# Performance work log

Measured on AMD Instinct MI355X. Metric: run time of the kernel, lower is better.

## Reference

```python
import jax, jax.numpy as jnp
import numpy as np

T, H, F, E, K = 4096, 2048, 1408, 8, 2  # tokens, hidden, intermediate, experts, top_k


def setup_inputs() -> dict:
    key = jax.random.key(0)
    k1, k2, k3, k4 = jax.random.split(key, 4)
    return {
        "hidden_states": jax.random.normal(k1, (T, H), dtype=jnp.float32),
        "router_logits": jax.random.normal(k2, (T, E), dtype=jnp.float32),
        # w1: (E, 2, H, F) where dim 1 = [gate_proj, up_proj]
        "w1": jax.random.normal(k3, (E, 2, H, F), dtype=jnp.float32) * 0.02,
        # w2: (E, F, H) down projection
        "w2": jax.random.normal(k4, (E, F, H), dtype=jnp.float32) * 0.02,
        "top_k": K,
    }


def reference(hidden_states, router_logits, w1, w2, top_k):
    # Router: softmax over all experts, then select top_k.
    # renormalize_topk_logits=False -> combine weights are the raw softmax probs.
    probs = jax.nn.softmax(router_logits, axis=-1)            # (T, E)
    topk_w, topk_ids = jax.lax.top_k(probs, top_k)            # (T, K) each

    num_experts = w1.shape[0]
    out = jnp.zeros_like(hidden_states)                       # (T, H)
    # Fixed small loop over experts (structurally distinct weight slices);
    # each expert's FFN is a dense GEMM over all tokens, masked by the
    # per-token combine coefficient (0 for tokens not routed to this expert).
    for e in range(num_experts):
        coef = jnp.sum(jnp.where(topk_ids == e, topk_w, 0.0), axis=-1)  # (T,)
        gate = hidden_states @ w1[e, 0]                       # (T, F)
        up = hidden_states @ w1[e, 1]                         # (T, F)
        h = jax.nn.silu(gate) * up                            # SwiGLU
        out = out + coef[:, None] * (h @ w2[e])               # (T, H)
    return out
```

## Files before the change

kernel.cpp:

```cpp
#include <hip/hip_runtime.h>
#include <stdint.h>

#define T_TOK 4096
#define HID   2048
#define FF    1408
#define NE    8

typedef __attribute__((ext_vector_type(8))) short short8;
typedef __attribute__((ext_vector_type(4))) float f32x4;
typedef __attribute__((ext_vector_type(4))) unsigned int u32x4;

__device__ inline unsigned short f2bf(float f) {
  uint32_t u = __builtin_bit_cast(uint32_t, f);
  u += 0x7fffu + ((u >> 16) & 1u);
  return (unsigned short)(u >> 16);
}

__device__ inline uint32_t cvt_pk(float a, float b) {
  uint32_t r;
  asm("v_cvt_pk_bf16_f32 %0, %1, %2" : "=v"(r) : "v"(a), "v"(b));
  return r;
}

__device__ inline void bar_top() {
  asm volatile("" ::: "memory");
  __builtin_amdgcn_s_barrier();
  asm volatile("" ::: "memory");
}
__device__ inline void bar_lds_ready() {
  asm volatile("s_waitcnt lgkmcnt(0)" ::: "memory");
  __builtin_amdgcn_s_barrier();
  asm volatile("" ::: "memory");
}

__global__ __launch_bounds__(256) void route_kernel(const float* __restrict__ logits,
                                                    int2* __restrict__ eids,
                                                    float2* __restrict__ ecfs) {
  int t = blockIdx.x * 256 + threadIdx.x;
  const float4* lp = (const float4*)(logits + (size_t)t * NE);
  float4 a = lp[0], b = lp[1];
  float l[8] = {a.x, a.y, a.z, a.w, b.x, b.y, b.z, b.w};
  float mx = l[0];
#pragma unroll
  for (int i = 1; i < 8; ++i) mx = fmaxf(mx, l[i]);
  float s = 0.f, p[8];
#pragma unroll
  for (int i = 0; i < 8; ++i) { p[i] = __expf(l[i] - mx); s += p[i]; }
  float inv = 1.f / s;
  int e0 = 0;
#pragma unroll
  for (int i = 1; i < 8; ++i) if (l[i] > l[e0]) e0 = i;
  int e1 = (e0 == 0) ? 1 : 0;
#pragma unroll
  for (int i = 0; i < 8; ++i) if (i != e0 && l[i] > l[e1]) e1 = i;
  eids[t] = make_int2(e0, e1);
  ecfs[t] = make_float2(p[e0] * inv, p[e1] * inv);
}

__global__ __launch_bounds__(256) void compact_kernel(const int2* __restrict__ eids,
                                                      const float2* __restrict__ ecfs,
                                                      int* __restrict__ tok,
                                                      float* __restrict__ coef,
                                                      int* __restrict__ rowptr) {
  int e = blockIdx.x, tid = threadIdx.x;
  __shared__ int hist[8];
  __shared__ int wsum[4];
  __shared__ int runv;
  if (tid < 8) hist[tid] = 0;
  __syncthreads();
  for (int t = tid; t < T_TOK; t += 256) {
    int2 ei = eids[t];
    atomicAdd(&hist[ei.x], 1);
    atomicAdd(&hist[ei.y], 1);
  }
  __syncthreads();
  int off = 0;
  for (int j = 0; j < e; ++j) off += hist[j];
  if (tid == 0) {
    runv = 0;
    if (e == 0) rowptr[0] = 0;
    rowptr[e + 1] = off + hist[e];
  }
  __syncthreads();
  int wave = tid >> 6, lane = tid & 63;
  for (int c = 0; c < T_TOK; c += 256) {
    int t = c + tid;
    int2 ei = eids[t];
    float2 cf = ecfs[t];
    bool fl = false; float cv = 0.f;
    if (ei.x == e)      { fl = true; cv = cf.x; }
    else if (ei.y == e) { fl = true; cv = cf.y; }
    unsigned long long m = __ballot(fl);
    if (lane == 0) wsum[wave] = __popcll(m);
    __syncthreads();
    int woff = runv;
    for (int wv = 0; wv < wave; ++wv) woff += wsum[wv];
    int pos = off + woff + __popcll(m & ((1ull << lane) - 1ull));
    if (fl) { tok[pos] = t; coef[pos] = cv; }
    __syncthreads();
    if (tid == 0) runv += wsum[0] + wsum[1] + wsum[2] + wsum[3];
    __syncthreads();
  }
}

__global__ __launch_bounds__(256) void cvtx_kernel(const float* __restrict__ x,
                                                   unsigned short* __restrict__ xb) {
  int i = blockIdx.x * 256 + threadIdx.x;
  float4 v = ((const float4*)x)[i];
  uint2 o;
  o.x = cvt_pk(v.x, v.y);
  o.y = cvt_pk(v.z, v.w);
  ((uint2*)xb)[i] = o;
}

__global__ __launch_bounds__(256) void gemm1_kernel(const unsigned short* __restrict__ Xb,
                                                    const float* __restrict__ w1,
                                                    const int* __restrict__ tok,
                                                    const int* __restrict__ rowptr,
                                                    unsigned short* __restrict__ hbuf) {
  int f = blockIdx.x + 22 * blockIdx.y;
  int g = (f & 7) * 88 + (f >> 3);
  int ftile = g >> 5, mtile = g & 31;
  int e = blockIdx.z;
  int base = rowptr[e], cnt = rowptr[e + 1] - base;
  if (mtile * 128 >= cnt) return;
  __shared__ char As[128 * 64];
  __shared__ char Bs[128 * 64];
  int tid = threadIdx.x, lane = tid & 63, wave = tid >> 6;

  int c = tid & 3, r0 = tid >> 2;
  int s0 = min(mtile * 128 + r0, cnt - 1);
  int s1 = min(mtile * 128 + 64 + r0, cnt - 1);
  const unsigned short* gA0 = Xb + (size_t)tok[base + s0] * HID + c * 8;
  const unsigned short* gA1 = Xb + (size_t)tok[base + s1] * HID + c * 8;
  int swzA = c ^ ((r0 >> 1) & 3);
  char* wA0 = As + r0 * 64 + (swzA << 4);
  char* wA1 = As + (64 + r0) * 64 + (swzA << 4);

  int bl = tid & 63, bw = tid >> 6;
  int n2 = bl * 2;
  int gsel = (n2 >= 64) ? 1 : 0;
  int fcol = ftile * 64 + (n2 & 63);
  const float* gB = w1 + ((size_t)(e * 2 + gsel) * HID + bw * 8) * FF + fcol;
  int swzB = bw ^ ((n2 >> 1) & 3);
  char* wB0 = Bs + n2 * 64 + (swzB << 4);
  char* wB1 = Bs + (n2 + 1) * 64 + (swzB << 4);

  int wm = wave >> 1, wf = wave & 1;
  int kc = lane >> 4;
  int aoff[4];
#pragma unroll
  for (int mi = 0; mi < 4; ++mi) {
    int row = wm * 64 + mi * 16 + (lane & 15);
    aoff[mi] = row * 64 + ((kc ^ ((row >> 1) & 3)) << 4);
  }
  int bgo[2];
#pragma unroll
  for (int ni = 0; ni < 2; ++ni) {
    int ng = wf * 32 + ni * 16 + (lane & 15);
    bgo[ni] = ng * 64 + ((kc ^ ((ng >> 1) & 3)) << 4);
  }

  const f32x4 vz = {0.f, 0.f, 0.f, 0.f};
  f32x4 accg[4][2], accu[4][2];
#pragma unroll
  for (int mi = 0; mi < 4; ++mi)
#pragma unroll
    for (int ni = 0; ni < 2; ++ni) { accg[mi][ni] = vz; accu[mi][ni] = vz; }

  short8 a0 = *(const short8*)gA0;
  short8 a1 = *(const short8*)gA1;
  float2 v[8];
#pragma unroll
  for (int dk = 0; dk < 8; ++dk) v[dk] = *(const float2*)(gB + (size_t)dk * FF);

  for (int k0 = 0; k0 < HID; k0 += 32) {
    int kn = (k0 + 32 < HID) ? k0 + 32 : k0;
    bar_top();
    u32x4 px, py;
#pragma unroll
    for (int j = 0; j < 4; ++j) {
      px[j] = cvt_pk(v[2 * j].x, v[2 * j + 1].x);
      py[j] = cvt_pk(v[2 * j].y, v[2 * j + 1].y);
    }
    *(short8*)wA0 = a0;
    *(short8*)wA1 = a1;
    *(u32x4*)wB0 = px;
    *(u32x4*)wB1 = py;
    a0 = *(const short8*)(gA0 + kn);
    a1 = *(const short8*)(gA1 + kn);
#pragma unroll
    for (int dk = 0; dk < 8; ++dk) v[dk] = *(const float2*)(gB + ((size_t)kn + dk) * FF);
    bar_lds_ready();
    short8 af[4];
#pragma unroll
    for (int mi = 0; mi < 4; ++mi) af[mi] = *(const short8*)(As + aoff[mi]);
    short8 bg[2], bu[2];
#pragma unroll
    for (int ni = 0; ni < 2; ++ni) {
      bg[ni] = *(const short8*)(Bs + bgo[ni]);
      bu[ni] = *(const short8*)(Bs + bgo[ni] + 64 * 64);
    }
#pragma unroll
    for (int mi = 0; mi < 4; ++mi)
#pragma unroll
      for (int ni = 0; ni < 2; ++ni) {
        accg[mi][ni] = __builtin_amdgcn_mfma_f32_16x16x32_bf16(af[mi], bg[ni], accg[mi][ni], 0, 0, 0);
        accu[mi][ni] = __builtin_amdgcn_mfma_f32_16x16x32_bf16(af[mi], bu[ni], accu[mi][ni], 0, 0, 0);
      }
  }
  int fb = ftile * 64 + wf * 32;
#pragma unroll
  for (int mi = 0; mi < 4; ++mi) {
#pragma unroll
    for (int i = 0; i < 4; ++i) {
      int ml = wm * 64 + mi * 16 + (lane >> 4) * 4 + i;
      int slot = mtile * 128 + ml;
      if (slot < cnt) {
#pragma unroll
        for (int ni = 0; ni < 2; ++ni) {
          float g = accg[mi][ni][i], u = accu[mi][ni][i];
          float hv = g / (1.f + __expf(-g)) * u;
          hbuf[(size_t)(base + slot) * FF + fb + ni * 16 + (lane & 15)] = f2bf(hv);
        }
      }
    }
  }
}

__global__ __launch_bounds__(256) void gemm2_kernel(const unsigned short* __restrict__ hbuf,
                                                    const float* __restrict__ w2,
                                                    const int* __restrict__ tok,
                                                    const float* __restrict__ coef,
                                                    const int* __restrict__ rowptr,
                                                    float* __restrict__ out) {
  int f = blockIdx.x + 16 * blockIdx.y;
  int g = (f & 7) * 64 + (f >> 3);
  int ntile = g >> 5, mtile = g & 31;
  int e = blockIdx.z;
  int base = rowptr[e], cnt = rowptr[e + 1] - base;
  if (mtile * 128 >= cnt) return;
  __shared__ char As[128 * 64];
  __shared__ char Bs[128 * 64];
  __shared__ int tokL[128];
  __shared__ float cofL[128];
  int tid = threadIdx.x, lane = tid & 63, wave = tid >> 6;
  if (tid < 128) {
    int slot = min(mtile * 128 + tid, cnt - 1);
    tokL[tid] = tok[base + slot];
    cofL[tid] = coef[base + slot];
  }
  __syncthreads();

  int c = tid & 3, r0 = tid >> 2;
  int s0 = min(mtile * 128 + r0, cnt - 1);
  int s1 = min(mtile * 128 + 64 + r0, cnt - 1);
  const unsigned short* gA0 = hbuf + (size_t)(base + s0) * FF + c * 8;
  const unsigned short* gA1 = hbuf + (size_t)(base + s1) * FF + c * 8;
  int swzA = c ^ ((r0 >> 1) & 3);
  char* wA0 = As + r0 * 64 + (swzA << 4);
  char* wA1 = As + (64 + r0) * 64 + (swzA << 4);

  int bl = tid & 63, bw = tid >> 6;
  int n2 = bl * 2;
  int ncol = ntile * 128 + n2;
  const float* gB = w2 + ((size_t)e * FF + bw * 8) * HID + ncol;
  int swzB = bw ^ ((n2 >> 1) & 3);
  char* wB0 = Bs + n2 * 64 + (swzB << 4);
  char* wB1 = Bs + (n2 + 1) * 64 + (swzB << 4);

  int wm = wave >> 1, wn = wave & 1;
  int kc = lane >> 4;
  int aoff[4], bo[4];
#pragma unroll
  for (int mi = 0; mi < 4; ++mi) {
    int row = wm * 64 + mi * 16 + (lane & 15);
    aoff[mi] = row * 64 + ((kc ^ ((row >> 1) & 3)) << 4);
  }
#pragma unroll
  for (int ni = 0; ni < 4; ++ni) {
    int n = wn * 64 + ni * 16 + (lane & 15);
    bo[ni] = n * 64 + ((kc ^ ((n >> 1) & 3)) << 4);
  }

  const f32x4 vz = {0.f, 0.f, 0.f, 0.f};
  f32x4 acc[4][4];
#pragma unroll
  for (int mi = 0; mi < 4; ++mi)
#pragma unroll
    for (int ni = 0; ni < 4; ++ni) acc[mi][ni] = vz;

  short8 a0 = *(const short8*)gA0;
  short8 a1 = *(const short8*)gA1;
  float2 v[8];
#pragma unroll
  for (int dk = 0; dk < 8; ++dk) v[dk] = *(const float2*)(gB + (size_t)dk * HID);

  for (int k0 = 0; k0 < FF; k0 += 32) {
    int kn = (k0 + 32 < FF) ? k0 + 32 : k0;
    bar_top();
    u32x4 px, py;
#pragma unroll
    for (int j = 0; j < 4; ++j) {
      px[j] = cvt_pk(v[2 * j].x, v[2 * j + 1].x);
      py[j] = cvt_pk(v[2 * j].y, v[2 * j + 1].y);
    }
    *(short8*)wA0 = a0;
    *(short8*)wA1 = a1;
    *(u32x4*)wB0 = px;
    *(u32x4*)wB1 = py;
    a0 = *(const short8*)(gA0 + kn);
    a1 = *(const short8*)(gA1 + kn);
#pragma unroll
    for (int dk = 0; dk < 8; ++dk) v[dk] = *(const float2*)(gB + ((size_t)kn + dk) * HID);
    bar_lds_ready();
    short8 af[4], bb[4];
#pragma unroll
    for (int mi = 0; mi < 4; ++mi) af[mi] = *(const short8*)(As + aoff[mi]);
#pragma unroll
    for (int ni = 0; ni < 4; ++ni) bb[ni] = *(const short8*)(Bs + bo[ni]);
#pragma unroll
    for (int mi = 0; mi < 4; ++mi)
#pragma unroll
      for (int ni = 0; ni < 4; ++ni)
        acc[mi][ni] = __builtin_amdgcn_mfma_f32_16x16x32_bf16(af[mi], bb[ni], acc[mi][ni], 0, 0, 0);
  }
#pragma unroll
  for (int mi = 0; mi < 4; ++mi) {
#pragma unroll
    for (int i = 0; i < 4; ++i) {
      int ml = wm * 64 + mi * 16 + (lane >> 4) * 4 + i;
      int slot = mtile * 128 + ml;
      if (slot < cnt) {
        float cf = cofL[ml];
        float* op = out + (size_t)tokL[ml] * HID + ntile * 128 + wn * 64 + (lane & 15);
#pragma unroll
        for (int ni = 0; ni < 4; ++ni)
          unsafeAtomicAdd(op + ni * 16, cf * acc[mi][ni][i]);
      }
    }
  }
}

extern "C" void kernel_launch(void* const* d_in, const int* in_sizes, int n_in,
                              void* d_out, int out_size, void* d_ws, size_t ws_size,
                              hipStream_t stream) {
  const float* X  = (const float*)d_in[0];
  const float* RL = (const float*)d_in[1];
  const float* W1 = (const float*)d_in[2];
  const float* W2 = (const float*)d_in[3];
  float* out = (float*)d_out;

  const size_t OFF_EIDS = 4096;
  const size_t OFF_ECFS = 36864;
  const size_t OFF_TOK  = 69632;
  const size_t OFF_COEF = 102400;
  const size_t OFF_XB   = 135168;
  const size_t OFF_H    = 16912384;
  const size_t TOTAL    = 39981056;
  if (ws_size < TOTAL || n_in < 4) return;

  char* w = (char*)d_ws;
  int*    rowptr = (int*)w;
  int2*   eids   = (int2*)(w + OFF_EIDS);
  float2* ecfs   = (float2*)(w + OFF_ECFS);
  int*    tok    = (int*)(w + OFF_TOK);
  float*  coef   = (float*)(w + OFF_COEF);
  unsigned short* Xb   = (unsigned short*)(w + OFF_XB);
  unsigned short* hbuf = (unsigned short*)(w + OFF_H);

  hipMemsetAsync(d_out, 0, (size_t)T_TOK * HID * sizeof(float), stream);
  route_kernel<<<T_TOK / 256, 256, 0, stream>>>(RL, eids, ecfs);
  compact_kernel<<<NE, 256, 0, stream>>>(eids, ecfs, tok, coef, rowptr);
  cvtx_kernel<<<(T_TOK * HID / 4) / 256, 256, 0, stream>>>(X, Xb);
  gemm1_kernel<<<dim3(FF / 64, T_TOK / 128, NE), 256, 0, stream>>>(Xb, W1, tok, rowptr, hbuf);
  gemm2_kernel<<<dim3(HID / 128, T_TOK / 128, NE), 256, 0, stream>>>(hbuf, W2, tok, coef, rowptr, out);
}
```

Before: 409.5 us.

## Pre-transpose and convert expert weights to bf16 before grouped GEMMs

Adds a kernel that converts the fp32 w1 and w2 weights to bf16 and transposes them into K-contiguous layouts in workspace every call. The GEMM kernels then load B tiles as 16-byte bf16 vectors, replacing strided fp32 float2 loads and the in-loop packing. gemm1 interleaves gate and up columns into a single 4x4 MFMA tile. The cost is an extra full pass over all weights (about 185 MB read, 92 MB written) per call, and the new path only runs when the workspace is large enough.

```diff
diff --git a/kernel.cpp b/kernel.cpp
--- a/kernel.cpp
+++ b/kernel.cpp
@@ -113,7 +113,232 @@
   ((uint2*)xb)[i] = o;
 }
 
+__global__ __launch_bounds__(256) void wcvt_kernel(const float* __restrict__ in,
+                                                   unsigned short* __restrict__ out,
+                                                   int R, int C) {
+  __shared__ unsigned short t[64][72];
+  const float* ip = in + ((size_t)blockIdx.z * R + blockIdx.y * 64) * C + blockIdx.x * 64;
+  int tid = threadIdx.x;
+  int r = tid >> 2, cg = (tid & 3) * 16;
+  const float* rp = ip + (size_t)r * C + cg;
+#pragma unroll
+  for (int j = 0; j < 4; ++j) {
+    float4 v = *(const float4*)(rp + j * 4);
+    int c = cg + j * 4;
+    t[c + 0][r] = f2bf(v.x);
+    t[c + 1][r] = f2bf(v.y);
+    t[c + 2][r] = f2bf(v.z);
+    t[c + 3][r] = f2bf(v.w);
+  }
+  __syncthreads();
+  int cr = tid >> 2, kg = (tid & 3) * 16;
+  unsigned short* op = out + ((size_t)blockIdx.z * C + blockIdx.x * 64 + cr) * R +
+                       blockIdx.y * 64 + kg;
+  *(short8*)op = *(const short8*)&t[cr][kg];
+  *(short8*)(op + 8) = *(const short8*)&t[cr][kg + 8];
+}
+
 __global__ __launch_bounds__(256) void gemm1_kernel(const unsigned short* __restrict__ Xb,
+                                                    const unsigned short* __restrict__ w1t,
+                                                    const int* __restrict__ tok,
+                                                    const int* __restrict__ rowptr,
+                                                    unsigned short* __restrict__ hbuf) {
+  int f = blockIdx.x + 22 * blockIdx.y;
+  int g = (f & 7) * 88 + (f >> 3);
+  int ftile = g >> 5, mtile = g & 31;
+  int e = blockIdx.z;
+  int base = rowptr[e], cnt = rowptr[e + 1] - base;
+  if (mtile * 128 >= cnt) return;
+  __shared__ char As[128 * 64];
+  __shared__ char Bs[128 * 64];
+  int tid = threadIdx.x, lane = tid & 63, wave = tid >> 6;
+
+  int c = tid & 3, r0 = tid >> 2;
+  int s0 = min(mtile * 128 + r0, cnt - 1);
+  int s1 = min(mtile * 128 + 64 + r0, cnt - 1);
+  const unsigned short* gA0 = Xb + (size_t)tok[base + s0] * HID + c * 8;
+  const unsigned short* gA1 = Xb + (size_t)tok[base + s1] * HID + c * 8;
+  int swz = c ^ ((r0 >> 1) & 3);
+  char* wA0 = As + r0 * 64 + (swz << 4);
+  char* wA1 = As + (64 + r0) * 64 + (swz << 4);
+
+  int proj = (r0 >> 4) & 1;
+  int fl = (r0 & 15) + 16 * (r0 >> 5);
+  const unsigned short* gB0 = w1t + ((size_t)(e * 2 + proj) * FF + ftile * 64 + fl) * HID + c * 8;
+  const unsigned short* gB1 = gB0 + (size_t)32 * HID;
+  char* wB0 = Bs + r0 * 64 + (swz << 4);
+  char* wB1 = Bs + (64 + r0) * 64 + (swz << 4);
+
+  int wm = wave >> 1, wn = wave & 1, kc = lane >> 4;
+  int aoff[4], boff[4];
+#pragma unroll
+  for (int mi = 0; mi < 4; ++mi) {
+    int row = wm * 64 + mi * 16 + (lane & 15);
+    aoff[mi] = row * 64 + ((kc ^ ((row >> 1) & 3)) << 4);
+  }
+#pragma unroll
+  for (int ni = 0; ni < 4; ++ni) {
+    int n = wn * 64 + ni * 16 + (lane & 15);
+    boff[ni] = n * 64 + ((kc ^ ((n >> 1) & 3)) << 4);
+  }
+
+  const f32x4 vz = {0.f, 0.f, 0.f, 0.f};
+  f32x4 acc[4][4];
+#pragma unroll
+  for (int mi = 0; mi < 4; ++mi)
+#pragma unroll
+    for (int ni = 0; ni < 4; ++ni) acc[mi][ni] = vz;
+
+  short8 a0 = *(const short8*)gA0;
+  short8 a1 = *(const short8*)gA1;
+  short8 b0 = *(const short8*)gB0;
+  short8 b1 = *(const short8*)gB1;
+
+  for (int k0 = 0; k0 < HID; k0 += 32) {
+    int kn = (k0 + 32 < HID) ? k0 + 32 : k0;
+    bar_top();
+    *(short8*)wA0 = a0;
+    *(short8*)wA1 = a1;
+    *(short8*)wB0 = b0;
+    *(short8*)wB1 = b1;
+    a0 = *(const short8*)(gA0 + kn);
+    a1 = *(const short8*)(gA1 + kn);
+    b0 = *(const short8*)(gB0 + kn);
+    b1 = *(const short8*)(gB1 + kn);
+    bar_lds_ready();
+    short8 af[4], bb[4];
+#pragma unroll
+    for (int mi = 0; mi < 4; ++mi) af[mi] = *(const short8*)(As + aoff[mi]);
+#pragma unroll
+    for (int ni = 0; ni < 4; ++ni) bb[ni] = *(const short8*)(Bs + boff[ni]);
+#pragma unroll
+    for (int mi = 0; mi < 4; ++mi)
+#pragma unroll
+      for (int ni = 0; ni < 4; ++ni)
+        acc[mi][ni] = __builtin_amdgcn_mfma_f32_16x16x32_bf16(af[mi], bb[ni], acc[mi][ni], 0, 0, 0);
+  }
+  int fb = ftile * 64 + wn * 32 + (lane & 15);
+#pragma unroll
+  for (int mi = 0; mi < 4; ++mi) {
+#pragma unroll
+    for (int i = 0; i < 4; ++i) {
+      int ml = wm * 64 + mi * 16 + (lane >> 4) * 4 + i;
+      int slot = mtile * 128 + ml;
+      if (slot < cnt) {
+        size_t hrow = (size_t)(base + slot) * FF + fb;
+        float g0 = acc[mi][0][i], u0 = acc[mi][1][i];
+        float g1 = acc[mi][2][i], u1 = acc[mi][3][i];
+        hbuf[hrow]      = f2bf(g0 / (1.f + __expf(-g0)) * u0);
+        hbuf[hrow + 16] = f2bf(g1 / (1.f + __expf(-g1)) * u1);
+      }
+    }
+  }
+}
+
+__global__ __launch_bounds__(256) void gemm2_kernel(const unsigned short* __restrict__ hbuf,
+                                                    const unsigned short* __restrict__ w2t,
+                                                    const int* __restrict__ tok,
+                                                    const float* __restrict__ coef,
+                                                    const int* __restrict__ rowptr,
+                                                    float* __restrict__ out) {
+  int f = blockIdx.x + 16 * blockIdx.y;
+  int g = (f & 7) * 64 + (f >> 3);
+  int ntile = g >> 5, mtile = g & 31;
+  int e = blockIdx.z;
+  int base = rowptr[e], cnt = rowptr[e + 1] - base;
+  if (mtile * 128 >= cnt) return;
+  __shared__ char As[128 * 64];
+  __shared__ char Bs[128 * 64];
+  __shared__ int tokL[128];
+  __shared__ float cofL[128];
+  int tid = threadIdx.x, lane = tid & 63, wave = tid >> 6;
+  if (tid < 128) {
+    int slot = min(mtile * 128 + tid, cnt - 1);
+    tokL[tid] = tok[base + slot];
+    cofL[tid] = coef[base + slot];
+  }
+  __syncthreads();
+
+  int c = tid & 3, r0 = tid >> 2;
+  int s0 = min(mtile * 128 + r0, cnt - 1);
+  int s1 = min(mtile * 128 + 64 + r0, cnt - 1);
+  const unsigned short* gA0 = hbuf + (size_t)(base + s0) * FF + c * 8;
+  const unsigned short* gA1 = hbuf + (size_t)(base + s1) * FF + c * 8;
+  int swz = c ^ ((r0 >> 1) & 3);
+  char* wA0 = As + r0 * 64 + (swz << 4);
+  char* wA1 = As + (64 + r0) * 64 + (swz << 4);
+
+  const unsigned short* gB0 = w2t + ((size_t)e * HID + ntile * 128 + r0) * FF + c * 8;
+  const unsigned short* gB1 = gB0 + (size_t)64 * FF;
+  char* wB0 = Bs + r0 * 64 + (swz << 4);
+  char* wB1 = Bs + (64 + r0) * 64 + (swz << 4);
+
+  int wm = wave >> 1, wn = wave & 1, kc = lane >> 4;
+  int aoff[4], boff[4];
+#pragma unroll
+  for (int mi = 0; mi < 4; ++mi) {
+    int row = wm * 64 + mi * 16 + (lane & 15);
+    aoff[mi] = row * 64 + ((kc ^ ((row >> 1) & 3)) << 4);
+  }
+#pragma unroll
+  for (int ni = 0; ni < 4; ++ni) {
+    int n = wn * 64 + ni * 16 + (lane & 15);
+    boff[ni] = n * 64 + ((kc ^ ((n >> 1) & 3)) << 4);
+  }
+
+  const f32x4 vz = {0.f, 0.f, 0.f, 0.f};
+  f32x4 acc[4][4];
+#pragma unroll
+  for (int mi = 0; mi < 4; ++mi)
+#pragma unroll
+    for (int ni = 0; ni < 4; ++ni) acc[mi][ni] = vz;
+
+  short8 a0 = *(const short8*)gA0;
+  short8 a1 = *(const short8*)gA1;
+  short8 b0 = *(const short8*)gB0;
+  short8 b1 = *(const short8*)gB1;
+
+  for (int k0 = 0; k0 < FF; k0 += 32) {
+    int kn = (k0 + 32 < FF) ? k0 + 32 : k0;
+    bar_top();
+    *(short8*)wA0 = a0;
+    *(short8*)wA1 = a1;
+    *(short8*)wB0 = b0;
+    *(short8*)wB1 = b1;
+    a0 = *(const short8*)(gA0 + kn);
+    a1 = *(const short8*)(gA1 + kn);
+    b0 = *(const short8*)(gB0 + kn);
+    b1 = *(const short8*)(gB1 + kn);
+    bar_lds_ready();
+    short8 af[4], bb[4];
+#pragma unroll
+    for (int mi = 0; mi < 4; ++mi) af[mi] = *(const short8*)(As + aoff[mi]);
+#pragma unroll
+    for (int ni = 0; ni < 4; ++ni) bb[ni] = *(const short8*)(Bs + boff[ni]);
+#pragma unroll
+    for (int mi = 0; mi < 4; ++mi)
+#pragma unroll
+      for (int ni = 0; ni < 4; ++ni)
+        acc[mi][ni] = __builtin_amdgcn_mfma_f32_16x16x32_bf16(af[mi], bb[ni], acc[mi][ni], 0, 0, 0);
+  }
+#pragma unroll
+  for (int mi = 0; mi < 4; ++mi) {
+#pragma unroll
+    for (int i = 0; i < 4; ++i) {
+      int ml = wm * 64 + mi * 16 + (lane >> 4) * 4 + i;
+      int slot = mtile * 128 + ml;
+      if (slot < cnt) {
+        float cf = cofL[ml];
+        float* op = out + (size_t)tokL[ml] * HID + ntile * 128 + wn * 64 + (lane & 15);
+#pragma unroll
+        for (int ni = 0; ni < 4; ++ni)
+          unsafeAtomicAdd(op + ni * 16, cf * acc[mi][ni][i]);
+      }
+    }
+  }
+}
+
+__global__ __launch_bounds__(256) void gemm1_legacy(const unsigned short* __restrict__ Xb,
                                                     const float* __restrict__ w1,
                                                     const int* __restrict__ tok,
                                                     const int* __restrict__ rowptr,
@@ -127,7 +352,6 @@
   __shared__ char As[128 * 64];
   __shared__ char Bs[128 * 64];
   int tid = threadIdx.x, lane = tid & 63, wave = tid >> 6;
-
   int c = tid & 3, r0 = tid >> 2;
   int s0 = min(mtile * 128 + r0, cnt - 1);
   int s1 = min(mtile * 128 + 64 + r0, cnt - 1);
@@ -136,7 +360,6 @@
   int swzA = c ^ ((r0 >> 1) & 3);
   char* wA0 = As + r0 * 64 + (swzA << 4);
   char* wA1 = As + (64 + r0) * 64 + (swzA << 4);
-
   int bl = tid & 63, bw = tid >> 6;
   int n2 = bl * 2;
   int gsel = (n2 >= 64) ? 1 : 0;
@@ -145,7 +368,6 @@
   int swzB = bw ^ ((n2 >> 1) & 3);
   char* wB0 = Bs + n2 * 64 + (swzB << 4);
   char* wB1 = Bs + (n2 + 1) * 64 + (swzB << 4);
-
   int wm = wave >> 1, wf = wave & 1;
   int kc = lane >> 4;
   int aoff[4];
@@ -160,20 +382,17 @@
     int ng = wf * 32 + ni * 16 + (lane & 15);
     bgo[ni] = ng * 64 + ((kc ^ ((ng >> 1) & 3)) << 4);
   }
-
   const f32x4 vz = {0.f, 0.f, 0.f, 0.f};
   f32x4 accg[4][2], accu[4][2];
 #pragma unroll
   for (int mi = 0; mi < 4; ++mi)
 #pragma unroll
     for (int ni = 0; ni < 2; ++ni) { accg[mi][ni] = vz; accu[mi][ni] = vz; }
-
   short8 a0 = *(const short8*)gA0;
   short8 a1 = *(const short8*)gA1;
   float2 v[8];
 #pragma unroll
   for (int dk = 0; dk < 8; ++dk) v[dk] = *(const float2*)(gB + (size_t)dk * FF);
-
   for (int k0 = 0; k0 < HID; k0 += 32) {
     int kn = (k0 + 32 < HID) ? k0 + 32 : k0;
     bar_top();
@@ -219,8 +438,8 @@
       if (slot < cnt) {
 #pragma unroll
         for (int ni = 0; ni < 2; ++ni) {
-          float g = accg[mi][ni][i], u = accu[mi][ni][i];
-          float hv = g / (1.f + __expf(-g)) * u;
+          float gg = accg[mi][ni][i], uu = accu[mi][ni][i];
+          float hv = gg / (1.f + __expf(-gg)) * uu;
           hbuf[(size_t)(base + slot) * FF + fb + ni * 16 + (lane & 15)] = f2bf(hv);
         }
       }
@@ -228,7 +447,7 @@
   }
 }
 
-__global__ __launch_bounds__(256) void gemm2_kernel(const unsigned short* __restrict__ hbuf,
+__global__ __launch_bounds__(256) void gemm2_legacy(const unsigned short* __restrict__ hbuf,
                                                     const float* __restrict__ w2,
                                                     const int* __restrict__ tok,
                                                     const float* __restrict__ coef,
@@ -251,7 +470,6 @@
     cofL[tid] = coef[base + slot];
   }
   __syncthreads();
-
   int c = tid & 3, r0 = tid >> 2;
   int s0 = min(mtile * 128 + r0, cnt - 1);
   int s1 = min(mtile * 128 + 64 + r0, cnt - 1);
@@ -260,7 +478,6 @@
   int swzA = c ^ ((r0 >> 1) & 3);
   char* wA0 = As + r0 * 64 + (swzA << 4);
   char* wA1 = As + (64 + r0) * 64 + (swzA << 4);
-
   int bl = tid & 63, bw = tid >> 6;
   int n2 = bl * 2;
   int ncol = ntile * 128 + n2;
@@ -268,7 +485,6 @@
   int swzB = bw ^ ((n2 >> 1) & 3);
   char* wB0 = Bs + n2 * 64 + (swzB << 4);
   char* wB1 = Bs + (n2 + 1) * 64 + (swzB << 4);
-
   int wm = wave >> 1, wn = wave & 1;
   int kc = lane >> 4;
   int aoff[4], bo[4];
@@ -282,20 +498,17 @@
     int n = wn * 64 + ni * 16 + (lane & 15);
     bo[ni] = n * 64 + ((kc ^ ((n >> 1) & 3)) << 4);
   }
-
   const f32x4 vz = {0.f, 0.f, 0.f, 0.f};
   f32x4 acc[4][4];
 #pragma unroll
   for (int mi = 0; mi < 4; ++mi)
 #pragma unroll
     for (int ni = 0; ni < 4; ++ni) acc[mi][ni] = vz;
-
   short8 a0 = *(const short8*)gA0;
   short8 a1 = *(const short8*)gA1;
   float2 v[8];
 #pragma unroll
   for (int dk = 0; dk < 8; ++dk) v[dk] = *(const float2*)(gB + (size_t)dk * HID);
-
   for (int k0 = 0; k0 < FF; k0 += 32) {
     int kn = (k0 + 32 < FF) ? k0 + 32 : k0;
     bar_top();
@@ -357,8 +570,11 @@
   const size_t OFF_COEF = 102400;
   const size_t OFF_XB   = 135168;
   const size_t OFF_H    = 16912384;
-  const size_t TOTAL    = 39981056;
-  if (ws_size < TOTAL || n_in < 4) return;
+  const size_t OFF_W1T  = 39981056;
+  const size_t OFF_W2T  = 132255744;
+  const size_t TOTAL1   = 39981056;
+  const size_t TOTAL2   = 178393088;
+  if (ws_size < TOTAL1 || n_in < 4) return;
 
   char* w = (char*)d_ws;
   int*    rowptr = (int*)w;
@@ -373,6 +589,16 @@
   route_kernel<<<T_TOK / 256, 256, 0, stream>>>(RL, eids, ecfs);
   compact_kernel<<<NE, 256, 0, stream>>>(eids, ecfs, tok, coef, rowptr);
   cvtx_kernel<<<(T_TOK * HID / 4) / 256, 256, 0, stream>>>(X, Xb);
-  gemm1_kernel<<<dim3(FF / 64, T_TOK / 128, NE), 256, 0, stream>>>(Xb, W1, tok, rowptr, hbuf);
-  gemm2_kernel<<<dim3(HID / 128, T_TOK / 128, NE), 256, 0, stream>>>(hbuf, W2, tok, coef, rowptr, out);
-}
+
+  if (ws_size >= TOTAL2) {
+    unsigned short* w1t = (unsigned short*)(w + OFF_W1T);
+    unsigned short* w2t = (unsigned short*)(w + OFF_W2T);
+    wcvt_kernel<<<dim3(FF / 64, HID / 64, NE * 2), 256, 0, stream>>>(W1, w1t, HID, FF);
+    wcvt_kernel<<<dim3(HID / 64, FF / 64, NE), 256, 0, stream>>>(W2, w2t, FF, HID);
+    gemm1_kernel<<<dim3(FF / 64, T_TOK / 128, NE), 256, 0, stream>>>(Xb, w1t, tok, rowptr, hbuf);
+    gemm2_kernel<<<dim3(HID / 128, T_TOK / 128, NE), 256, 0, stream>>>(hbuf, w2t, tok, coef, rowptr, out);
+  } else {
+    gemm1_legacy<<<dim3(FF / 64, T_TOK / 128, NE), 256, 0, stream>>>(Xb, W1, tok, rowptr, hbuf);
+    gemm2_legacy<<<dim3(HID / 128, T_TOK / 128, NE), 256, 0, stream>>>(hbuf, W2, tok, coef, rowptr, out);
+  }
+}
```

Measured after the change: 377.5 us. 1.08x faster.

## Pre-transpose weights to bf16 and double-buffer GEMM tiles via global_load_lds

Applied to the files above, without the earlier changes.

Adds a kernel that converts and transposes w1 and w2 to bf16 K-contiguous layouts in the workspace on every call. Both GEMMs then stream A and B tiles straight into double-buffered LDS with global_load_lds, which removes the in-loop fp32-to-bf16 conversion, the register staging and one barrier per iteration. In exchange the weights take an extra full read and write pass each call, and the workspace requirement grows substantially.

```diff
diff --git a/kernel.cpp b/kernel.cpp
--- a/kernel.cpp
+++ b/kernel.cpp
@@ -8,7 +8,6 @@
 
 typedef __attribute__((ext_vector_type(8))) short short8;
 typedef __attribute__((ext_vector_type(4))) float f32x4;
-typedef __attribute__((ext_vector_type(4))) unsigned int u32x4;
 
 __device__ inline unsigned short f2bf(float f) {
   uint32_t u = __builtin_bit_cast(uint32_t, f);
@@ -22,13 +21,14 @@
   return r;
 }
 
-__device__ inline void bar_top() {
-  asm volatile("" ::: "memory");
-  __builtin_amdgcn_s_barrier();
-  asm volatile("" ::: "memory");
-}
-__device__ inline void bar_lds_ready() {
-  asm volatile("s_waitcnt lgkmcnt(0)" ::: "memory");
+__device__ inline void gload16(const void* g, void* l) {
+  __builtin_amdgcn_global_load_lds(
+      (const __attribute__((address_space(1))) unsigned int*)g,
+      (__attribute__((address_space(3))) unsigned int*)l, 16, 0, 0);
+}
+
+__device__ inline void vm0_barrier() {
+  asm volatile("s_waitcnt vmcnt(0)" ::: "memory");
   __builtin_amdgcn_s_barrier();
   asm volatile("" ::: "memory");
 }
@@ -113,8 +113,33 @@
   ((uint2*)xb)[i] = o;
 }
 
+__global__ __launch_bounds__(256) void wcvt_kernel(const float* __restrict__ in,
+                                                   unsigned short* __restrict__ out,
+                                                   int R, int C) {
+  __shared__ unsigned short t[64][72];
+  const float* ip = in + ((size_t)blockIdx.z * R + blockIdx.y * 64) * C + blockIdx.x * 64;
+  int tid = threadIdx.x;
+  int r = tid >> 2, cg = (tid & 3) * 16;
+  const float* rp = ip + (size_t)r * C + cg;
+#pragma unroll
+  for (int j = 0; j < 4; ++j) {
+    float4 v = *(const float4*)(rp + j * 4);
+    int c = cg + j * 4;
+    t[c + 0][r] = f2bf(v.x);
+    t[c + 1][r] = f2bf(v.y);
+    t[c + 2][r] = f2bf(v.z);
+    t[c + 3][r] = f2bf(v.w);
+  }
+  __syncthreads();
+  int cr = tid >> 2, kg = (tid & 3) * 16;
+  unsigned short* op = out + ((size_t)blockIdx.z * C + blockIdx.x * 64 + cr) * R +
+                       blockIdx.y * 64 + kg;
+  *(short8*)op = *(const short8*)&t[cr][kg];
+  *(short8*)(op + 8) = *(const short8*)&t[cr][kg + 8];
+}
+
 __global__ __launch_bounds__(256) void gemm1_kernel(const unsigned short* __restrict__ Xb,
-                                                    const float* __restrict__ w1,
+                                                    const unsigned short* __restrict__ w1t,
                                                     const int* __restrict__ tok,
                                                     const int* __restrict__ rowptr,
                                                     unsigned short* __restrict__ hbuf) {
@@ -124,92 +149,72 @@
   int e = blockIdx.z;
   int base = rowptr[e], cnt = rowptr[e + 1] - base;
   if (mtile * 128 >= cnt) return;
-  __shared__ char As[128 * 64];
-  __shared__ char Bs[128 * 64];
+  __shared__ char As[2][8192];
+  __shared__ char Bs[2][8192];
   int tid = threadIdx.x, lane = tid & 63, wave = tid >> 6;
 
-  int c = tid & 3, r0 = tid >> 2;
-  int s0 = min(mtile * 128 + r0, cnt - 1);
-  int s1 = min(mtile * 128 + 64 + r0, cnt - 1);
-  const unsigned short* gA0 = Xb + (size_t)tok[base + s0] * HID + c * 8;
-  const unsigned short* gA1 = Xb + (size_t)tok[base + s1] * HID + c * 8;
-  int swzA = c ^ ((r0 >> 1) & 3);
-  char* wA0 = As + r0 * 64 + (swzA << 4);
-  char* wA1 = As + (64 + r0) * 64 + (swzA << 4);
-
-  int bl = tid & 63, bw = tid >> 6;
-  int n2 = bl * 2;
-  int gsel = (n2 >= 64) ? 1 : 0;
-  int fcol = ftile * 64 + (n2 & 63);
-  const float* gB = w1 + ((size_t)(e * 2 + gsel) * HID + bw * 8) * FF + fcol;
-  int swzB = bw ^ ((n2 >> 1) & 3);
-  char* wB0 = Bs + n2 * 64 + (swzB << 4);
-  char* wB1 = Bs + (n2 + 1) * 64 + (swzB << 4);
-
-  int wm = wave >> 1, wf = wave & 1;
-  int kc = lane >> 4;
-  int aoff[4];
+  int rA = wave * 32 + (lane >> 2);
+  int cd = (lane & 3) ^ ((rA >> 1) & 3);
+  int sA0 = min(mtile * 128 + rA, cnt - 1);
+  int sA1 = min(mtile * 128 + rA + 16, cnt - 1);
+  const unsigned short* gA0 = Xb + (size_t)tok[base + sA0] * HID + cd * 8;
+  const unsigned short* gA1 = Xb + (size_t)tok[base + sA1] * HID + cd * 8;
+  int r1 = rA + 16;
+  int p0 = (rA >> 4) & 1, f0 = (rA & 15) + 16 * (rA >> 5);
+  int p1 = (r1 >> 4) & 1, f1 = (r1 & 15) + 16 * (r1 >> 5);
+  const unsigned short* gB0 = w1t + ((size_t)(e * 2 + p0) * FF + ftile * 64 + f0) * HID + cd * 8;
+  const unsigned short* gB1 = w1t + ((size_t)(e * 2 + p1) * FF + ftile * 64 + f1) * HID + cd * 8;
+  int lb = wave * 2048;
+
+#define STAGE1(buf, k0) do {                       \
+    gload16(gA0 + (k0), As[buf] + lb);             \
+    gload16(gA1 + (k0), As[buf] + lb + 1024);      \
+    gload16(gB0 + (k0), Bs[buf] + lb);             \
+    gload16(gB1 + (k0), Bs[buf] + lb + 1024);      \
+  } while (0)
+
+  int wm = wave >> 1, wn = wave & 1, kc = lane >> 4;
+  int aoff[4], boff[4];
 #pragma unroll
   for (int mi = 0; mi < 4; ++mi) {
     int row = wm * 64 + mi * 16 + (lane & 15);
     aoff[mi] = row * 64 + ((kc ^ ((row >> 1) & 3)) << 4);
   }
-  int bgo[2];
-#pragma unroll
-  for (int ni = 0; ni < 2; ++ni) {
-    int ng = wf * 32 + ni * 16 + (lane & 15);
-    bgo[ni] = ng * 64 + ((kc ^ ((ng >> 1) & 3)) << 4);
+#pragma unroll
+  for (int ni = 0; ni < 4; ++ni) {
+    int n = wn * 64 + ni * 16 + (lane & 15);
+    boff[ni] = n * 64 + ((kc ^ ((n >> 1) & 3)) << 4);
   }
 
   const f32x4 vz = {0.f, 0.f, 0.f, 0.f};
-  f32x4 accg[4][2], accu[4][2];
+  f32x4 acc[4][4];
 #pragma unroll
   for (int mi = 0; mi < 4; ++mi)
 #pragma unroll
-    for (int ni = 0; ni < 2; ++ni) { accg[mi][ni] = vz; accu[mi][ni] = vz; }
-
-  short8 a0 = *(const short8*)gA0;
-  short8 a1 = *(const short8*)gA1;
-  float2 v[8];
-#pragma unroll
-  for (int dk = 0; dk < 8; ++dk) v[dk] = *(const float2*)(gB + (size_t)dk * FF);
-
-  for (int k0 = 0; k0 < HID; k0 += 32) {
-    int kn = (k0 + 32 < HID) ? k0 + 32 : k0;
-    bar_top();
-    u32x4 px, py;
-#pragma unroll
-    for (int j = 0; j < 4; ++j) {
-      px[j] = cvt_pk(v[2 * j].x, v[2 * j + 1].x);
-      py[j] = cvt_pk(v[2 * j].y, v[2 * j + 1].y);
-    }
-    *(short8*)wA0 = a0;
-    *(short8*)wA1 = a1;
-    *(u32x4*)wB0 = px;
-    *(u32x4*)wB1 = py;
-    a0 = *(const short8*)(gA0 + kn);
-    a1 = *(const short8*)(gA1 + kn);
-#pragma unroll
-    for (int dk = 0; dk < 8; ++dk) v[dk] = *(const float2*)(gB + ((size_t)kn + dk) * FF);
-    bar_lds_ready();
-    short8 af[4];
-#pragma unroll
-    for (int mi = 0; mi < 4; ++mi) af[mi] = *(const short8*)(As + aoff[mi]);
-    short8 bg[2], bu[2];
-#pragma unroll
-    for (int ni = 0; ni < 2; ++ni) {
-      bg[ni] = *(const short8*)(Bs + bgo[ni]);
-      bu[ni] = *(const short8*)(Bs + bgo[ni] + 64 * 64);
-    }
+    for (int ni = 0; ni < 4; ++ni) acc[mi][ni] = vz;
+
+  STAGE1(0, 0);
+  vm0_barrier();
+#pragma unroll 2
+  for (int it = 0; it < HID / 32; ++it) {
+    int cur = it & 1;
+    int k0 = it * 32;
+    if (it + 1 < HID / 32) STAGE1(cur ^ 1, k0 + 32);
+    short8 af[4], bb[4];
+#pragma unroll
+    for (int mi = 0; mi < 4; ++mi) af[mi] = *(const short8*)(As[cur] + aoff[mi]);
+#pragma unroll
+    for (int ni = 0; ni < 4; ++ni) bb[ni] = *(const short8*)(Bs[cur] + boff[ni]);
 #pragma unroll
     for (int mi = 0; mi < 4; ++mi)
 #pragma unroll
-      for (int ni = 0; ni < 2; ++ni) {
-        accg[mi][ni] = __builtin_amdgcn_mfma_f32_16x16x32_bf16(af[mi], bg[ni], accg[mi][ni], 0, 0, 0);
-        accu[mi][ni] = __builtin_amdgcn_mfma_f32_16x16x32_bf16(af[mi], bu[ni], accu[mi][ni], 0, 0, 0);
-      }
-  }
-  int fb = ftile * 64 + wf * 32;
+      for (int ni = 0; ni < 4; ++ni)
+        acc[mi][ni] = __builtin_amdgcn_mfma_f32_16x16x32_bf16(af[mi], bb[ni], acc[mi][ni], 0, 0, 0);
+    vm0_barrier();
+  }
+#undef STAGE1
+
+  int fb = ftile * 64 + wn * 32 + (lane & 15);
 #pragma unroll
   for (int mi = 0; mi < 4; ++mi) {
 #pragma unroll
@@ -217,19 +222,18 @@
       int ml = wm * 64 + mi * 16 + (lane >> 4) * 4 + i;
       int slot = mtile * 128 + ml;
       if (slot < cnt) {
-#pragma unroll
-        for (int ni = 0; ni < 2; ++ni) {
-          float g = accg[mi][ni][i], u = accu[mi][ni][i];
-          float hv = g / (1.f + __expf(-g)) * u;
-          hbuf[(size_t)(base + slot) * FF + fb + ni * 16 + (lane & 15)] = f2bf(hv);
-        }
+        size_t hrow = (size_t)(base + slot) * FF + fb;
+        float g0 = acc[mi][0][i], u0 = acc[mi][1][i];
+        float g1 = acc[mi][2][i], u1 = acc[mi][3][i];
+        hbuf[hrow]      = f2bf(g0 / (1.f + __expf(-g0)) * u0);
+        hbuf[hrow + 16] = f2bf(g1 / (1.f + __expf(-g1)) * u1);
       }
     }
   }
 }
 
 __global__ __launch_bounds__(256) void gemm2_kernel(const unsigned short* __restrict__ hbuf,
-                                                    const float* __restrict__ w2,
+                                                    const unsigned short* __restrict__ w2t,
                                                     const int* __restrict__ tok,
                                                     const float* __restrict__ coef,
                                                     const int* __restrict__ rowptr,
@@ -240,8 +244,8 @@
   int e = blockIdx.z;
   int base = rowptr[e], cnt = rowptr[e + 1] - base;
   if (mtile * 128 >= cnt) return;
-  __shared__ char As[128 * 64];
-  __shared__ char Bs[128 * 64];
+  __shared__ char As[2][8192];
+  __shared__ char Bs[2][8192];
   __shared__ int tokL[128];
   __shared__ float cofL[128];
   int tid = threadIdx.x, lane = tid & 63, wave = tid >> 6;
@@ -252,26 +256,25 @@
   }
   __syncthreads();
 
-  int c = tid & 3, r0 = tid >> 2;
-  int s0 = min(mtile * 128 + r0, cnt - 1);
-  int s1 = min(mtile * 128 + 64 + r0, cnt - 1);
-  const unsigned short* gA0 = hbuf + (size_t)(base + s0) * FF + c * 8;
-  const unsigned short* gA1 = hbuf + (size_t)(base + s1) * FF + c * 8;
-  int swzA = c ^ ((r0 >> 1) & 3);
-  char* wA0 = As + r0 * 64 + (swzA << 4);
-  char* wA1 = As + (64 + r0) * 64 + (swzA << 4);
-
-  int bl = tid & 63, bw = tid >> 6;
-  int n2 = bl * 2;
-  int ncol = ntile * 128 + n2;
-  const float* gB = w2 + ((size_t)e * FF + bw * 8) * HID + ncol;
-  int swzB = bw ^ ((n2 >> 1) & 3);
-  char* wB0 = Bs + n2 * 64 + (swzB << 4);
-  char* wB1 = Bs + (n2 + 1) * 64 + (swzB << 4);
-
-  int wm = wave >> 1, wn = wave & 1;
-  int kc = lane >> 4;
-  int aoff[4], bo[4];
+  int rA = wave * 32 + (lane >> 2);
+  int cd = (lane & 3) ^ ((rA >> 1) & 3);
+  int sA0 = min(mtile * 128 + rA, cnt - 1);
+  int sA1 = min(mtile * 128 + rA + 16, cnt - 1);
+  const unsigned short* gA0 = hbuf + (size_t)(base + sA0) * FF + cd * 8;
+  const unsigned short* gA1 = hbuf + (size_t)(base + sA1) * FF + cd * 8;
+  const unsigned short* gB0 = w2t + ((size_t)e * HID + ntile * 128 + rA) * FF + cd * 8;
+  const unsigned short* gB1 = gB0 + (size_t)16 * FF;
+  int lb = wave * 2048;
+
+#define STAGE2(buf, k0) do {                       \
+    gload16(gA0 + (k0), As[buf] + lb);             \
+    gload16(gA1 + (k0), As[buf] + lb + 1024);      \
+    gload16(gB0 + (k0), Bs[buf] + lb);             \
+    gload16(gB1 + (k0), Bs[buf] + lb + 1024);      \
+  } while (0)
+
+  int wm = wave >> 1, wn = wave & 1, kc = lane >> 4;
+  int aoff[4], boff[4];
 #pragma unroll
   for (int mi = 0; mi < 4; ++mi) {
     int row = wm * 64 + mi * 16 + (lane & 15);
@@ -280,7 +283,7 @@
 #pragma unroll
   for (int ni = 0; ni < 4; ++ni) {
     int n = wn * 64 + ni * 16 + (lane & 15);
-    bo[ni] = n * 64 + ((kc ^ ((n >> 1) & 3)) << 4);
+    boff[ni] = n * 64 + ((kc ^ ((n >> 1) & 3)) << 4);
   }
 
   const f32x4 vz = {0.f, 0.f, 0.f, 0.f};
@@ -290,41 +293,27 @@
 #pragma unroll
     for (int ni = 0; ni < 4; ++ni) acc[mi][ni] = vz;
 
-  short8 a0 = *(const short8*)gA0;
-  short8 a1 = *(const short8*)gA1;
-  float2 v[8];
-#pragma unroll
-  for (int dk = 0; dk < 8; ++dk) v[dk] = *(const float2*)(gB + (size_t)dk * HID);
-
-  for (int k0 = 0; k0 < FF; k0 += 32) {
-    int kn = (k0 + 32 < FF) ? k0 + 32 : k0;
-    bar_top();
-    u32x4 px, py;
-#pragma unroll
-    for (int j = 0; j < 4; ++j) {
-      px[j] = cvt_pk(v[2 * j].x, v[2 * j + 1].x);
-      py[j] = cvt_pk(v[2 * j].y, v[2 * j + 1].y);
-    }
-    *(short8*)wA0 = a0;
-    *(short8*)wA1 = a1;
-    *(u32x4*)wB0 = px;
-    *(u32x4*)wB1 = py;
-    a0 = *(const short8*)(gA0 + kn);
-    a1 = *(const short8*)(gA1 + kn);
-#pragma unroll
-    for (int dk = 0; dk < 8; ++dk) v[dk] = *(const float2*)(gB + ((size_t)kn + dk) * HID);
-    bar_lds_ready();
+  STAGE2(0, 0);
+  vm0_barrier();
+#pragma unroll 2
+  for (int it = 0; it < FF / 32; ++it) {
+    int cur = it & 1;
+    int k0 = it * 32;
+    if (it + 1 < FF / 32) STAGE2(cur ^ 1, k0 + 32);
     short8 af[4], bb[4];
 #pragma unroll
-    for (int mi = 0; mi < 4; ++mi) af[mi] = *(const short8*)(As + aoff[mi]);
-#pragma unroll
-    for (int ni = 0; ni < 4; ++ni) bb[ni] = *(const short8*)(Bs + bo[ni]);
+    for (int mi = 0; mi < 4; ++mi) af[mi] = *(const short8*)(As[cur] + aoff[mi]);
+#pragma unroll
+    for (int ni = 0; ni < 4; ++ni) bb[ni] = *(const short8*)(Bs[cur] + boff[ni]);
 #pragma unroll
     for (int mi = 0; mi < 4; ++mi)
 #pragma unroll
       for (int ni = 0; ni < 4; ++ni)
         acc[mi][ni] = __builtin_amdgcn_mfma_f32_16x16x32_bf16(af[mi], bb[ni], acc[mi][ni], 0, 0, 0);
-  }
+    vm0_barrier();
+  }
+#undef STAGE2
+
 #pragma unroll
   for (int mi = 0; mi < 4; ++mi) {
 #pragma unroll
@@ -357,8 +346,10 @@
   const size_t OFF_COEF = 102400;
   const size_t OFF_XB   = 135168;
   const size_t OFF_H    = 16912384;
-  const size_t TOTAL    = 39981056;
-  if (ws_size < TOTAL || n_in < 4) return;
+  const size_t OFF_W1T  = 39981056;
+  const size_t OFF_W2T  = 132255744;
+  const size_t TOTAL2   = 178393088;
+  if (ws_size < TOTAL2 || n_in < 4) return;
 
   char* w = (char*)d_ws;
   int*    rowptr = (int*)w;
@@ -368,11 +359,15 @@
   float*  coef   = (float*)(w + OFF_COEF);
   unsigned short* Xb   = (unsigned short*)(w + OFF_XB);
   unsigned short* hbuf = (unsigned short*)(w + OFF_H);
+  unsigned short* w1t  = (unsigned short*)(w + OFF_W1T);
+  unsigned short* w2t  = (unsigned short*)(w + OFF_W2T);
 
   hipMemsetAsync(d_out, 0, (size_t)T_TOK * HID * sizeof(float), stream);
   route_kernel<<<T_TOK / 256, 256, 0, stream>>>(RL, eids, ecfs);
   compact_kernel<<<NE, 256, 0, stream>>>(eids, ecfs, tok, coef, rowptr);
   cvtx_kernel<<<(T_TOK * HID / 4) / 256, 256, 0, stream>>>(X, Xb);
-  gemm1_kernel<<<dim3(FF / 64, T_TOK / 128, NE), 256, 0, stream>>>(Xb, W1, tok, rowptr, hbuf);
-  gemm2_kernel<<<dim3(HID / 128, T_TOK / 128, NE), 256, 0, stream>>>(hbuf, W2, tok, coef, rowptr, out);
-}
+  wcvt_kernel<<<dim3(FF / 64, HID / 64, NE * 2), 256, 0, stream>>>(W1, w1t, HID, FF);
+  wcvt_kernel<<<dim3(HID / 64, FF / 64, NE), 256, 0, stream>>>(W2, w2t, FF, HID);
+  gemm1_kernel<<<dim3(FF / 64, T_TOK / 128, NE), 256, 0, stream>>>(Xb, w1t, tok, rowptr, hbuf);
+  gemm2_kernel<<<dim3(HID / 128, T_TOK / 128, NE), 256, 0, stream>>>(hbuf, w2t, tok, coef, rowptr, out);
+}
```

Measured after the change: 400.4 us. 1.02x faster.
